# Optimization experiments

Measured on AMD Instinct MI355X. Metric: run time of the kernel, lower is better.

## Reference

```python
import jax, jax.numpy as jnp
import numpy as np

THRESH = 0.3
DECAY = 0.5


def spike_fn(x):
    # Heaviside threshold (forward only)
    return (x > THRESH).astype(x.dtype)


def setup_inputs() -> dict:
    key = jax.random.key(0)
    k_in, k0, k1, k2 = jax.random.split(key, 4)
    B, D0, T = 128, 512, 512
    inputs = jax.random.uniform(k_in, (B, D0, T), dtype=jnp.float32)
    w0 = jax.random.normal(k0, (512, 1024), dtype=jnp.float32)
    w1 = jax.random.normal(k1, (1024, 1024), dtype=jnp.float32)
    w2 = jax.random.normal(k2, (1024, 512), dtype=jnp.float32)
    return {"inputs": inputs, "w0": w0, "w1": w1, "w2": w2}


def reference(inputs, w0, w1, w2):
    ws = (w0, w1, w2)
    B = inputs.shape[0]
    layer_dims = tuple(w.shape[1] for w in ws)

    # time-major: [T, B, D0]
    xs = jnp.transpose(inputs, (2, 0, 1))

    mem0 = tuple(jnp.zeros((B, d), dtype=inputs.dtype) for d in layer_dims)
    spk0 = tuple(jnp.zeros((B, d), dtype=inputs.dtype) for d in layer_dims)

    def step(carry, x_t):
        mems, spikes = carry
        prev_spike = x_t  # layer-0 spikes come straight from the input
        new_mems, new_spikes = [], []
        for i, w in enumerate(ws):
            # leaky integrate with reset-by-spike, then fire
            mem = mems[i] * DECAY * (1.0 - spikes[i]) + prev_spike @ w
            s = spike_fn(mem)
            new_mems.append(mem)
            new_spikes.append(s)
            prev_spike = s
        return (tuple(new_mems), tuple(new_spikes)), None

    (_, spikes_final), _ = jax.lax.scan(step, (mem0, spk0), xs)
    return spikes_final[-1]
```

## Files before the change

kernel.cpp:

```cpp
#include <hip/hip_runtime.h>


typedef __bf16 bf16;
typedef __attribute__((ext_vector_type(8))) __bf16 bf16x8;
typedef __attribute__((ext_vector_type(16))) float f32x16;
typedef unsigned long long u64;

#define B_   128
#define D0_  512
#define T_   512
#define TS_  128
#define N1_  1024
#define N2_  1024
#define N3_  512
#define MFMA32(a,b,c) __builtin_amdgcn_mfma_f32_32x32x16_bf16((a),(b),(c),0,0,0)

#define GL2LDS(g, l) __builtin_amdgcn_global_load_lds( \
    (const __attribute__((address_space(1))) void*)(g), \
    (__attribute__((address_space(3))) void*)(l), 16, 0, 0)


__global__ __launch_bounds__(256)
void split_w(const float* __restrict__ W, bf16* __restrict__ WTh, bf16* __restrict__ WTl,
             int K, int N)
{
    __shared__ float tile[32][33];
    const int k0 = blockIdx.x * 32, n0 = blockIdx.y * 32;
    const int tx = threadIdx.x & 31, ty = threadIdx.x >> 5;
#pragma unroll
    for (int r = 0; r < 4; ++r)
        tile[ty + r * 8][tx] = W[(size_t)(k0 + ty + r * 8) * N + n0 + tx];
    __syncthreads();
#pragma unroll
    for (int r = 0; r < 4; ++r) {
        int nl = ty + r * 8;
        float v = tile[tx][nl];
        bf16 h = (bf16)v;
        size_t o = (size_t)(n0 + nl) * K + k0 + tx;
        WTh[o] = h;
        WTl[o] = (bf16)(v - (float)h);
    }
}

__global__ __launch_bounds__(256)
void split_x(const float* __restrict__ in, bf16* __restrict__ Xh, bf16* __restrict__ Xl)
{
    __shared__ float tile[32][33];
    const int b = blockIdx.z, d0 = blockIdx.x * 32, t0 = blockIdx.y * 32;
    const int tx = threadIdx.x & 31, ty = threadIdx.x >> 5;
#pragma unroll
    for (int r = 0; r < 4; ++r)
        tile[ty + r * 8][tx] = in[((size_t)b * D0_ + d0 + ty + r * 8) * T_ + t0 + tx];
    __syncthreads();
    const int s = t0 >> 7;
#pragma unroll
    for (int r = 0; r < 4; ++r) {
        int t  = t0 + ty + r * 8;
        int tl = t & (TS_ - 1);
        float v = tile[tx][ty + r * 8];
        bf16 h = (bf16)v;
        size_t o = (((size_t)s * B_ + b) * TS_ + tl) * D0_ + d0 + tx;
        Xh[o] = h;
        Xl[o] = (bf16)(v - (float)h);
    }
}

__device__ __forceinline__ bf16x8 expand8(unsigned v)
{
    union { unsigned u[4]; bf16x8 h; } r;
#pragma unroll
    for (int i = 0; i < 4; ++i) {
        r.u[i] = (((v >> (2 * i)) & 1u) ? 0x3F80u : 0u) |
                 (((v >> (2 * i + 1)) & 1u) ? 0x3F800000u : 0u);
    }
    return r.h;
}

__global__ __launch_bounds__(256)
void snn_layer0(const bf16* __restrict__ Ah, const bf16* __restrict__ Al,
                const bf16* __restrict__ WTh, const bf16* __restrict__ WTl,
                u64* __restrict__ bitsOut)
{
    constexpr int K = D0_;
    __shared__ char smem[32768];
    bf16* sAh = (bf16*)smem;
    bf16* sAl = (bf16*)(smem + 8192);
    bf16* sBh = (bf16*)(smem + 16384);
    bf16* sBl = (bf16*)(smem + 24576);
    float* If = (float*)smem;

    const int tid = threadIdx.x, lane = tid & 63, w = tid >> 6;
    const int wm = w & 1, wn = w >> 1;
    const int l31 = lane & 31, kh = lane >> 5;
    const int b = blockIdx.x;
    const int nb = blockIdx.y * 128;

    const int i4 = lane >> 2, c4 = lane & 3;
    const int csrc = c4 ^ ((i4 >> 1) & 3);
    const bf16* gBh = WTh + (size_t)(nb + w * 32 + i4) * K + csrc * 8;
    const bf16* gBl = WTl + (size_t)(nb + w * 32 + i4) * K + csrc * 8;
    bf16* lA  = sAh + w * 32 * 32;
    bf16* lAl = sAl + w * 32 * 32;
    bf16* lBh = sBh + w * 32 * 32;
    bf16* lBl = sBl + w * 32 * 32;

    int rA[2], rB[2], swA[2], swB[2];
#pragma unroll
    for (int i = 0; i < 2; ++i) {
        rA[i] = wm * 64 + i * 32 + l31;
        rB[i] = wn * 64 + i * 32 + l31;
        swA[i] = (rA[i] >> 1) & 3;
        swB[i] = (rB[i] >> 1) & 3;
    }

    float cm = 0.f, cs = 0.f;
    const int scol = tid & 63;
    float* Ifb = If + (tid >> 6) * 4096;

#pragma unroll 1
    for (int s = 0; s < T_ / TS_; ++s) {
        const size_t arow = ((size_t)s * B_ + b) * TS_;
        const bf16* gA  = Ah + (arow + w * 32 + i4) * K + csrc * 8;
        const bf16* gAl = Al + (arow + w * 32 + i4) * K + csrc * 8;

        f32x16 acc[2][2] = {};

#pragma unroll 1
        for (int ks = 0; ks < K / 32; ++ks) {
            const int go = ks * 32;
            __syncthreads();
#pragma unroll
            for (int inst = 0; inst < 2; ++inst) {
                GL2LDS(gA  + (size_t)inst * 16 * K + go, lA  + inst * 16 * 32);
                GL2LDS(gAl + (size_t)inst * 16 * K + go, lAl + inst * 16 * 32);
                GL2LDS(gBh + (size_t)inst * 16 * K + go, lBh + inst * 16 * 32);
                GL2LDS(gBl + (size_t)inst * 16 * K + go, lBl + inst * 16 * 32);
            }
            __syncthreads();

            bf16x8 a[2][2], al2[2][2];
#pragma unroll
            for (int mi = 0; mi < 2; ++mi)
#pragma unroll
                for (int h = 0; h < 2; ++h) {
                    const int off = rA[mi] * 32 + (((2 * h + kh) ^ swA[mi]) * 8);
                    a[mi][h]   = *(const bf16x8*)(sAh + off);
                    al2[mi][h] = *(const bf16x8*)(sAl + off);
                }
#pragma unroll
            for (int ni = 0; ni < 2; ++ni) {
#pragma unroll
                for (int h = 0; h < 2; ++h) {
                    const int off = rB[ni] * 32 + (((2 * h + kh) ^ swB[ni]) * 8);
                    bf16x8 bh = *(const bf16x8*)(sBh + off);
                    bf16x8 bl = *(const bf16x8*)(sBl + off);
#pragma unroll
                    for (int mi = 0; mi < 2; ++mi) {
                        acc[mi][ni] = MFMA32(a[mi][h], bh, acc[mi][ni]);
                        acc[mi][ni] = MFMA32(al2[mi][h], bh, acc[mi][ni]);
                        acc[mi][ni] = MFMA32(a[mi][h], bl, acc[mi][ni]);
                    }
                }
            }
        }

        u64 word0 = 0, word1 = 0;
        __syncthreads();
        if (wm == 0) {
#pragma unroll
            for (int ni = 0; ni < 2; ++ni)
#pragma unroll
                for (int mi = 0; mi < 2; ++mi)
#pragma unroll
                    for (int r = 0; r < 16; ++r) {
                        const int tt = mi * 32 + (r & 3) + 8 * (r >> 2) + 4 * kh;
                        If[wn * 4096 + tt * 64 + ni * 32 + l31] = acc[mi][ni][r];
                    }
        }
        __syncthreads();
        if (tid < 128) {
            float m = cm, sp = cs;
#pragma unroll 4
            for (int tt = 0; tt < 64; ++tt) {
                m = m * 0.5f * (1.0f - sp) + Ifb[tt * 64 + scol];
                const bool fire = m > 0.3f;
                sp = fire ? 1.0f : 0.0f;
                u64 bal = __ballot(fire);
                if ((tid & 63) == tt) word0 = bal;
            }
            cm = m; cs = sp;
        }
        __syncthreads();
        if (wm == 1) {
#pragma unroll
            for (int ni = 0; ni < 2; ++ni)
#pragma unroll
                for (int mi = 0; mi < 2; ++mi)
#pragma unroll
                    for (int r = 0; r < 16; ++r) {
                        const int tt = mi * 32 + (r & 3) + 8 * (r >> 2) + 4 * kh;
                        If[wn * 4096 + tt * 64 + ni * 32 + l31] = acc[mi][ni][r];
                    }
        }
        __syncthreads();
        if (tid < 128) {
            float m = cm, sp = cs;
#pragma unroll 4
            for (int tt = 0; tt < 64; ++tt) {
                m = m * 0.5f * (1.0f - sp) + Ifb[tt * 64 + scol];
                const bool fire = m > 0.3f;
                sp = fire ? 1.0f : 0.0f;
                u64 bal = __ballot(fire);
                if ((tid & 63) == tt) word1 = bal;
            }
            cm = m; cs = sp;
            u64* dst = bitsOut + ((size_t)s * B_ + b) * 2048;
            const int j8 = (nb >> 6) + (tid >> 6);
            const int t0 = tid & 63, t1 = 64 + (tid & 63);
            dst[t0 * 16 + (j8 ^ (t0 & 15))] = word0;
            dst[t1 * 16 + (j8 ^ (t1 & 15))] = word1;
        }
    }
}

template<bool WRITE_BITS>
__global__ __launch_bounds__(256, 3)
void snn_layer_bits(const u64* __restrict__ bitsIn,
                    const bf16* __restrict__ WTh, const bf16* __restrict__ WTl,
                    u64* __restrict__ bitsOut, float* __restrict__ outp, int N)
{
    constexpr int K = 1024;
    __shared__ char smem[49152];
    char* bitsLds = smem;
    bf16* sBh = (bf16*)(smem + 16384);
    bf16* sBl = (bf16*)(smem + 32768);
    float* If  = (float*)(smem + 16384);

    const int tid = threadIdx.x, lane = tid & 63, w = tid >> 6;
    const int wm = w & 1, wn = w >> 1;
    const int l31 = lane & 31, kh = lane >> 5;
    const int b = blockIdx.x;
    const int nb = blockIdx.y * 128;

    const int i8 = lane >> 3, c8 = lane & 7;
    const bf16* gBh = WTh + (size_t)(nb + w * 32 + i8) * K + (c8 ^ i8) * 8;
    const bf16* gBl = WTl + (size_t)(nb + w * 32 + i8) * K + (c8 ^ i8) * 8;
    bf16* lBh = sBh + (w * 32) * 64;
    bf16* lBl = sBl + (w * 32) * 64;

    int rA[2], rB[2];
#pragma unroll
    for (int i = 0; i < 2; ++i) {
        rA[i] = wm * 64 + i * 32 + l31;
        rB[i] = wn * 64 + i * 32 + l31;
    }
    const int sw7 = l31 & 7, sw15 = l31 & 15;

    float cm = 0.f, cs = 0.f;
    const int scol = tid & 63;
    float* Ifb = If + (tid >> 6) * 4096;

#pragma unroll 1
    for (int s = 0; s < T_ / TS_; ++s) {
        {
            const char* src = (const char*)bitsIn + ((size_t)s * B_ + b) * 16384;
#pragma unroll
            for (int i = 0; i < 4; ++i)
                GL2LDS(src + (w * 4 + i) * 1024 + lane * 16,
                       bitsLds + (w * 4 + i) * 1024);
        }

        f32x16 acc[2][2] = {};

#pragma unroll 1
        for (int ks = 0; ks < K / 64; ++ks) {
            const int go = ks * 64;
            __syncthreads();
#pragma unroll
            for (int inst = 0; inst < 4; ++inst) {
                GL2LDS(gBh + (size_t)(inst * 8) * K + go, lBh + inst * 8 * 64);
                GL2LDS(gBl + (size_t)(inst * 8) * K + go, lBl + inst * 8 * 64);
            }
            __syncthreads();

            u64 wA0 = *(const u64*)(bitsLds + rA[0] * 128 + ((ks ^ sw15) << 3)) >> (8 * kh);
            u64 wA1 = *(const u64*)(bitsLds + rA[1] * 128 + ((ks ^ sw15) << 3)) >> (8 * kh);

#pragma unroll
            for (int h = 0; h < 4; ++h) {
                bf16x8 a0 = expand8((unsigned)(wA0 >> (16 * h)) & 0xFFu);
                bf16x8 a1 = expand8((unsigned)(wA1 >> (16 * h)) & 0xFFu);
#pragma unroll
                for (int ni = 0; ni < 2; ++ni) {
                    const int off = rB[ni] * 64 + (((2 * h + kh) ^ sw7) << 3);
                    bf16x8 bh = *(const bf16x8*)(sBh + off);
                    bf16x8 bl = *(const bf16x8*)(sBl + off);
                    acc[0][ni] = MFMA32(a0, bh, acc[0][ni]);
                    acc[0][ni] = MFMA32(a0, bl, acc[0][ni]);
                    acc[1][ni] = MFMA32(a1, bh, acc[1][ni]);
                    acc[1][ni] = MFMA32(a1, bl, acc[1][ni]);
                }
            }
        }

        u64 word0 = 0, word1 = 0;
        __syncthreads();
        if (wm == 0) {
#pragma unroll
            for (int ni = 0; ni < 2; ++ni)
#pragma unroll
                for (int mi = 0; mi < 2; ++mi)
#pragma unroll
                    for (int r = 0; r < 16; ++r) {
                        const int tt = mi * 32 + (r & 3) + 8 * (r >> 2) + 4 * kh;
                        If[wn * 4096 + tt * 64 + ni * 32 + l31] = acc[mi][ni][r];
                    }
        }
        __syncthreads();
        if (tid < 128) {
            float m = cm, sp = cs;
#pragma unroll 4
            for (int tt = 0; tt < 64; ++tt) {
                m = m * 0.5f * (1.0f - sp) + Ifb[tt * 64 + scol];
                const bool fire = m > 0.3f;
                sp = fire ? 1.0f : 0.0f;
                if constexpr (WRITE_BITS) {
                    u64 bal = __ballot(fire);
                    if ((tid & 63) == tt) word0 = bal;
                }
            }
            cm = m; cs = sp;
        }
        __syncthreads();
        if (wm == 1) {
#pragma unroll
            for (int ni = 0; ni < 2; ++ni)
#pragma unroll
                for (int mi = 0; mi < 2; ++mi)
#pragma unroll
                    for (int r = 0; r < 16; ++r) {
                        const int tt = mi * 32 + (r & 3) + 8 * (r >> 2) + 4 * kh;
                        If[wn * 4096 + tt * 64 + ni * 32 + l31] = acc[mi][ni][r];
                    }
        }
        __syncthreads();
        if (tid < 128) {
            float m = cm, sp = cs;
#pragma unroll 4
            for (int tt = 0; tt < 64; ++tt) {
                m = m * 0.5f * (1.0f - sp) + Ifb[tt * 64 + scol];
                const bool fire = m > 0.3f;
                sp = fire ? 1.0f : 0.0f;
                if constexpr (WRITE_BITS) {
                    u64 bal = __ballot(fire);
                    if ((tid & 63) == tt) word1 = bal;
                }
            }
            cm = m; cs = sp;
            if constexpr (WRITE_BITS) {
                u64* dst = bitsOut + ((size_t)s * B_ + b) * 2048;
                const int j8 = (nb >> 6) + (tid >> 6);
                const int t0 = tid & 63, t1 = 64 + (tid & 63);
                dst[t0 * 16 + (j8 ^ (t0 & 15))] = word0;
                dst[t1 * 16 + (j8 ^ (t1 & 15))] = word1;
            } else {
                if (s == T_ / TS_ - 1)
                    outp[(size_t)b * N + nb + tid] = cs;
            }
        }
    }
}

extern "C" void kernel_launch(void* const* d_in, const int* in_sizes, int n_in,
                              void* d_out, int out_size, void* d_ws, size_t ws_size,
                              hipStream_t stream)
{
    const float* x  = (const float*)d_in[0];
    const float* w0 = (const float*)d_in[1];
    const float* w1 = (const float*)d_in[2];
    const float* w2 = (const float*)d_in[3];
    float* out = (float*)d_out;

    char* p = (char*)d_ws;
    bf16* w0h = (bf16*)p;  p += (size_t)N1_ * D0_ * 2;
    bf16* w0l = (bf16*)p;  p += (size_t)N1_ * D0_ * 2;
    bf16* w1h = (bf16*)p;  p += (size_t)N2_ * N1_ * 2;
    bf16* w1l = (bf16*)p;  p += (size_t)N2_ * N1_ * 2;
    bf16* w2h = (bf16*)p;  p += (size_t)N3_ * N2_ * 2;
    bf16* w2l = (bf16*)p;  p += (size_t)N3_ * N2_ * 2;
    bf16* Xh  = (bf16*)p;  p += (size_t)T_ * B_ * D0_ * 2;
    bf16* Xl  = (bf16*)p;  p += (size_t)T_ * B_ * D0_ * 2;
    u64* bits0 = (u64*)p;  p += (size_t)(T_/TS_) * B_ * TS_ * (N1_/8);
    u64* bits1 = (u64*)p;  p += (size_t)(T_/TS_) * B_ * TS_ * (N2_/8);

    split_w<<<dim3(D0_/32, N1_/32), 256, 0, stream>>>(w0, w0h, w0l, D0_, N1_);
    split_w<<<dim3(N1_/32, N2_/32), 256, 0, stream>>>(w1, w1h, w1l, N1_, N2_);
    split_w<<<dim3(N2_/32, N3_/32), 256, 0, stream>>>(w2, w2h, w2l, N2_, N3_);
    split_x<<<dim3(D0_/32, T_/32, B_), 256, 0, stream>>>(x, Xh, Xl);

    snn_layer0<<<dim3(B_, N1_/128), 256, 0, stream>>>(Xh, Xl, w0h, w0l, bits0);
    snn_layer_bits<true ><<<dim3(B_, N2_/128), 256, 0, stream>>>(
        bits0, w1h, w1l, bits1, nullptr, N2_);
    snn_layer_bits<false><<<dim3(B_, N3_/128), 256, 0, stream>>>(
        bits1, w2h, w2l, nullptr, out, N3_);
}
```

Baseline: 823.1 us.

## Double-buffer LDS tiles in layer GEMM kernels and simplify bit expansion

Converts the K-loops of the layer-0 and bit-input layer kernels to double-buffered LDS staging. The next tile's global-to-LDS loads are issued before the MFMAs on the current tile, so memory latency overlaps with compute and each step needs one barrier instead of two. Shared memory per block doubles (64KB and 80KB), and launch bounds drop occupancy to 2 blocks per CU. The spike-bit expansion into bf16 vectors is also rewritten as a multiply-and-mask trick instead of per-bit selects.

Result: faster. 804.2 us (-2.3%).

```diff
diff --git a/kernel.cpp b/kernel.cpp
--- a/kernel.cpp
+++ b/kernel.cpp
@@ -19,6 +19,10 @@
     (const __attribute__((address_space(1))) void*)(g), \
     (__attribute__((address_space(3))) void*)(l), 16, 0, 0)
 
+#define WAIT_BARRIER() do { \
+    asm volatile("s_waitcnt vmcnt(0)" ::: "memory"); \
+    __builtin_amdgcn_s_barrier(); } while (0)
+
 
 __global__ __launch_bounds__(256)
 void split_w(const float* __restrict__ W, bf16* __restrict__ WTh, bf16* __restrict__ WTl,
@@ -68,26 +72,29 @@
 __device__ __forceinline__ bf16x8 expand8(unsigned v)
 {
     union { unsigned u[4]; bf16x8 h; } r;
-#pragma unroll
-    for (int i = 0; i < 4; ++i) {
-        r.u[i] = (((v >> (2 * i)) & 1u) ? 0x3F80u : 0u) |
-                 (((v >> (2 * i + 1)) & 1u) ? 0x3F800000u : 0u);
-    }
+    const unsigned p = v * 0x8001u;
+#pragma unroll
+    for (int i = 0; i < 4; ++i)
+        r.u[i] = ((p >> (2 * i)) & 0x10001u) * 0x3F80u;
     return r.h;
 }
 
-__global__ __launch_bounds__(256)
+__global__ __launch_bounds__(256, 2)
 void snn_layer0(const bf16* __restrict__ Ah, const bf16* __restrict__ Al,
                 const bf16* __restrict__ WTh, const bf16* __restrict__ WTl,
                 u64* __restrict__ bitsOut)
 {
     constexpr int K = D0_;
-    __shared__ char smem[32768];
-    bf16* sAh = (bf16*)smem;
-    bf16* sAl = (bf16*)(smem + 8192);
-    bf16* sBh = (bf16*)(smem + 16384);
-    bf16* sBl = (bf16*)(smem + 24576);
-    float* If = (float*)smem;
+    __shared__ char smem[65536];
+    bf16* sA0  = (bf16*)(smem);
+    bf16* sAl0 = (bf16*)(smem + 8192);
+    bf16* sB0  = (bf16*)(smem + 16384);
+    bf16* sBl0 = (bf16*)(smem + 24576);
+    bf16* sA1  = (bf16*)(smem + 32768);
+    bf16* sAl1 = (bf16*)(smem + 40960);
+    bf16* sB1  = (bf16*)(smem + 49152);
+    bf16* sBl1 = (bf16*)(smem + 57344);
+    float* If  = (float*)smem;
 
     const int tid = threadIdx.x, lane = tid & 63, w = tid >> 6;
     const int wm = w & 1, wn = w >> 1;
@@ -99,10 +106,7 @@
     const int csrc = c4 ^ ((i4 >> 1) & 3);
     const bf16* gBh = WTh + (size_t)(nb + w * 32 + i4) * K + csrc * 8;
     const bf16* gBl = WTl + (size_t)(nb + w * 32 + i4) * K + csrc * 8;
-    bf16* lA  = sAh + w * 32 * 32;
-    bf16* lAl = sAl + w * 32 * 32;
-    bf16* lBh = sBh + w * 32 * 32;
-    bf16* lBl = sBl + w * 32 * 32;
+    const int wT = w * 32 * 32;
 
     int rA[2], rB[2], swA[2], swB[2];
 #pragma unroll
@@ -117,55 +121,67 @@
     const int scol = tid & 63;
     float* Ifb = If + (tid >> 6) * 4096;
 
+#define STAGE0(dA, dAl, dBh, dBl, go)                                          \
+    do {                                                                       \
+        _Pragma("unroll")                                                      \
+        for (int inst = 0; inst < 2; ++inst) {                                 \
+            GL2LDS(gA  + (size_t)(inst * 16) * K + (go), (dA)  + wT + inst * 16 * 32); \
+            GL2LDS(gAl + (size_t)(inst * 16) * K + (go), (dAl) + wT + inst * 16 * 32); \
+            GL2LDS(gBh + (size_t)(inst * 16) * K + (go), (dBh) + wT + inst * 16 * 32); \
+            GL2LDS(gBl + (size_t)(inst * 16) * K + (go), (dBl) + wT + inst * 16 * 32); \
+        }                                                                      \
+    } while (0)
+
+#define KSTEP0(cA, cAl, cBh, cBl)                                              \
+    do {                                                                       \
+        bf16x8 a[2][2], al2[2][2];                                             \
+        _Pragma("unroll")                                                      \
+        for (int mi = 0; mi < 2; ++mi)                                         \
+            _Pragma("unroll")                                                  \
+            for (int h = 0; h < 2; ++h) {                                      \
+                const int off = rA[mi] * 32 + (((2 * h + kh) ^ swA[mi]) * 8);  \
+                a[mi][h]   = *(const bf16x8*)((cA) + off);                     \
+                al2[mi][h] = *(const bf16x8*)((cAl) + off);                    \
+            }                                                                  \
+        _Pragma("unroll")                                                      \
+        for (int ni = 0; ni < 2; ++ni) {                                       \
+            _Pragma("unroll")                                                  \
+            for (int h = 0; h < 2; ++h) {                                      \
+                const int off = rB[ni] * 32 + (((2 * h + kh) ^ swB[ni]) * 8);  \
+                bf16x8 bh = *(const bf16x8*)((cBh) + off);                     \
+                bf16x8 bl = *(const bf16x8*)((cBl) + off);                     \
+                _Pragma("unroll")                                              \
+                for (int mi = 0; mi < 2; ++mi) {                               \
+                    acc[mi][ni] = MFMA32(a[mi][h], bh, acc[mi][ni]);           \
+                    acc[mi][ni] = MFMA32(al2[mi][h], bh, acc[mi][ni]);         \
+                    acc[mi][ni] = MFMA32(a[mi][h], bl, acc[mi][ni]);           \
+                }                                                              \
+            }                                                                  \
+        }                                                                      \
+        WAIT_BARRIER();                                                        \
+    } while (0)
+
 #pragma unroll 1
     for (int s = 0; s < T_ / TS_; ++s) {
         const size_t arow = ((size_t)s * B_ + b) * TS_;
         const bf16* gA  = Ah + (arow + w * 32 + i4) * K + csrc * 8;
         const bf16* gAl = Al + (arow + w * 32 + i4) * K + csrc * 8;
 
+        STAGE0(sA0, sAl0, sB0, sBl0, 0);
+        WAIT_BARRIER();
+
         f32x16 acc[2][2] = {};
 
 #pragma unroll 1
-        for (int ks = 0; ks < K / 32; ++ks) {
-            const int go = ks * 32;
-            __syncthreads();
-#pragma unroll
-            for (int inst = 0; inst < 2; ++inst) {
-                GL2LDS(gA  + (size_t)inst * 16 * K + go, lA  + inst * 16 * 32);
-                GL2LDS(gAl + (size_t)inst * 16 * K + go, lAl + inst * 16 * 32);
-                GL2LDS(gBh + (size_t)inst * 16 * K + go, lBh + inst * 16 * 32);
-                GL2LDS(gBl + (size_t)inst * 16 * K + go, lBl + inst * 16 * 32);
-            }
-            __syncthreads();
-
-            bf16x8 a[2][2], al2[2][2];
-#pragma unroll
-            for (int mi = 0; mi < 2; ++mi)
-#pragma unroll
-                for (int h = 0; h < 2; ++h) {
-                    const int off = rA[mi] * 32 + (((2 * h + kh) ^ swA[mi]) * 8);
-                    a[mi][h]   = *(const bf16x8*)(sAh + off);
-                    al2[mi][h] = *(const bf16x8*)(sAl + off);
-                }
-#pragma unroll
-            for (int ni = 0; ni < 2; ++ni) {
-#pragma unroll
-                for (int h = 0; h < 2; ++h) {
-                    const int off = rB[ni] * 32 + (((2 * h + kh) ^ swB[ni]) * 8);
-                    bf16x8 bh = *(const bf16x8*)(sBh + off);
-                    bf16x8 bl = *(const bf16x8*)(sBl + off);
-#pragma unroll
-                    for (int mi = 0; mi < 2; ++mi) {
-                        acc[mi][ni] = MFMA32(a[mi][h], bh, acc[mi][ni]);
-                        acc[mi][ni] = MFMA32(al2[mi][h], bh, acc[mi][ni]);
-                        acc[mi][ni] = MFMA32(a[mi][h], bl, acc[mi][ni]);
-                    }
-                }
-            }
+        for (int ks = 0; ks < K / 32; ks += 2) {
+            STAGE0(sA1, sAl1, sB1, sBl1, (ks + 1) * 32);
+            KSTEP0(sA0, sAl0, sB0, sBl0);
+            if (ks + 2 < K / 32)
+                STAGE0(sA0, sAl0, sB0, sBl0, (ks + 2) * 32);
+            KSTEP0(sA1, sAl1, sB1, sBl1);
         }
 
         u64 word0 = 0, word1 = 0;
-        __syncthreads();
         if (wm == 0) {
 #pragma unroll
             for (int ni = 0; ni < 2; ++ni)
@@ -220,20 +236,25 @@
             dst[t0 * 16 + (j8 ^ (t0 & 15))] = word0;
             dst[t1 * 16 + (j8 ^ (t1 & 15))] = word1;
         }
-    }
+        __syncthreads();
+    }
+#undef STAGE0
+#undef KSTEP0
 }
 
 template<bool WRITE_BITS>
-__global__ __launch_bounds__(256, 3)
+__global__ __launch_bounds__(256, 2)
 void snn_layer_bits(const u64* __restrict__ bitsIn,
                     const bf16* __restrict__ WTh, const bf16* __restrict__ WTl,
                     u64* __restrict__ bitsOut, float* __restrict__ outp, int N)
 {
     constexpr int K = 1024;
-    __shared__ char smem[49152];
+    __shared__ char smem[81920];
     char* bitsLds = smem;
-    bf16* sBh = (bf16*)(smem + 16384);
-    bf16* sBl = (bf16*)(smem + 32768);
+    bf16* sBh0 = (bf16*)(smem + 16384);
+    bf16* sBl0 = (bf16*)(smem + 32768);
+    bf16* sBh1 = (bf16*)(smem + 49152);
+    bf16* sBl1 = (bf16*)(smem + 65536);
     float* If  = (float*)(smem + 16384);
 
     const int tid = threadIdx.x, lane = tid & 63, w = tid >> 6;
@@ -245,8 +266,7 @@
     const int i8 = lane >> 3, c8 = lane & 7;
     const bf16* gBh = WTh + (size_t)(nb + w * 32 + i8) * K + (c8 ^ i8) * 8;
     const bf16* gBl = WTl + (size_t)(nb + w * 32 + i8) * K + (c8 ^ i8) * 8;
-    bf16* lBh = sBh + (w * 32) * 64;
-    bf16* lBl = sBl + (w * 32) * 64;
+    const int wB = w * 32 * 64;
 
     int rA[2], rB[2];
 #pragma unroll
@@ -254,11 +274,42 @@
         rA[i] = wm * 64 + i * 32 + l31;
         rB[i] = wn * 64 + i * 32 + l31;
     }
-    const int sw7 = l31 & 7, sw15 = l31 & 15;
+    const int sw7 = l31 & 7, sw15 = l31 & 15, sh8 = 8 * kh;
 
     float cm = 0.f, cs = 0.f;
     const int scol = tid & 63;
     float* Ifb = If + (tid >> 6) * 4096;
+
+#define STAGEB(dBh, dBl, go)                                                   \
+    do {                                                                       \
+        _Pragma("unroll")                                                      \
+        for (int inst = 0; inst < 4; ++inst) {                                 \
+            GL2LDS(gBh + (size_t)(inst * 8) * K + (go), (dBh) + wB + inst * 8 * 64); \
+            GL2LDS(gBl + (size_t)(inst * 8) * K + (go), (dBl) + wB + inst * 8 * 64); \
+        }                                                                      \
+    } while (0)
+
+#define KSTEPB(ks, cBh, cBl)                                                   \
+    do {                                                                       \
+        u64 wA0 = *(const u64*)(bitsLds + rA[0] * 128 + (((ks) ^ sw15) << 3)) >> sh8; \
+        u64 wA1 = *(const u64*)(bitsLds + rA[1] * 128 + (((ks) ^ sw15) << 3)) >> sh8; \
+        _Pragma("unroll")                                                      \
+        for (int h = 0; h < 4; ++h) {                                          \
+            bf16x8 a0 = expand8((unsigned)(wA0 >> (16 * h)) & 0xFFu);          \
+            bf16x8 a1 = expand8((unsigned)(wA1 >> (16 * h)) & 0xFFu);          \
+            _Pragma("unroll")                                                  \
+            for (int ni = 0; ni < 2; ++ni) {                                   \
+                const int off = rB[ni] * 64 + (((2 * h + kh) ^ sw7) << 3);     \
+                bf16x8 bh = *(const bf16x8*)((cBh) + off);                     \
+                bf16x8 bl = *(const bf16x8*)((cBl) + off);                     \
+                acc[0][ni] = MFMA32(a0, bh, acc[0][ni]);                       \
+                acc[0][ni] = MFMA32(a0, bl, acc[0][ni]);                       \
+                acc[1][ni] = MFMA32(a1, bh, acc[1][ni]);                       \
+                acc[1][ni] = MFMA32(a1, bl, acc[1][ni]);                       \
+            }                                                                  \
+        }                                                                      \
+        WAIT_BARRIER();                                                        \
+    } while (0)
 
 #pragma unroll 1
     for (int s = 0; s < T_ / TS_; ++s) {
@@ -269,42 +320,21 @@
                 GL2LDS(src + (w * 4 + i) * 1024 + lane * 16,
                        bitsLds + (w * 4 + i) * 1024);
         }
+        STAGEB(sBh0, sBl0, 0);
+        WAIT_BARRIER();
 
         f32x16 acc[2][2] = {};
 
 #pragma unroll 1
-        for (int ks = 0; ks < K / 64; ++ks) {
-            const int go = ks * 64;
-            __syncthreads();
-#pragma unroll
-            for (int inst = 0; inst < 4; ++inst) {
-                GL2LDS(gBh + (size_t)(inst * 8) * K + go, lBh + inst * 8 * 64);
-                GL2LDS(gBl + (size_t)(inst * 8) * K + go, lBl + inst * 8 * 64);
-            }
-            __syncthreads();
-
-            u64 wA0 = *(const u64*)(bitsLds + rA[0] * 128 + ((ks ^ sw15) << 3)) >> (8 * kh);
-            u64 wA1 = *(const u64*)(bitsLds + rA[1] * 128 + ((ks ^ sw15) << 3)) >> (8 * kh);
-
-#pragma unroll
-            for (int h = 0; h < 4; ++h) {
-                bf16x8 a0 = expand8((unsigned)(wA0 >> (16 * h)) & 0xFFu);
-                bf16x8 a1 = expand8((unsigned)(wA1 >> (16 * h)) & 0xFFu);
-#pragma unroll
-                for (int ni = 0; ni < 2; ++ni) {
-                    const int off = rB[ni] * 64 + (((2 * h + kh) ^ sw7) << 3);
-                    bf16x8 bh = *(const bf16x8*)(sBh + off);
-                    bf16x8 bl = *(const bf16x8*)(sBl + off);
-                    acc[0][ni] = MFMA32(a0, bh, acc[0][ni]);
-                    acc[0][ni] = MFMA32(a0, bl, acc[0][ni]);
-                    acc[1][ni] = MFMA32(a1, bh, acc[1][ni]);
-                    acc[1][ni] = MFMA32(a1, bl, acc[1][ni]);
-                }
-            }
+        for (int ks = 0; ks < K / 64; ks += 2) {
+            STAGEB(sBh1, sBl1, (ks + 1) * 64);
+            KSTEPB(ks, sBh0, sBl0);
+            if (ks + 2 < K / 64)
+                STAGEB(sBh0, sBl0, (ks + 2) * 64);
+            KSTEPB(ks + 1, sBh1, sBl1);
         }
 
         u64 word0 = 0, word1 = 0;
-        __syncthreads();
         if (wm == 0) {
 #pragma unroll
             for (int ni = 0; ni < 2; ++ni)
@@ -368,7 +398,10 @@
                     outp[(size_t)b * N + nb + tid] = cs;
             }
         }
-    }
+        __syncthreads();
+    }
+#undef STAGEB
+#undef KSTEPB
 }
 
 extern "C" void kernel_launch(void* const* d_in, const int* in_sizes, int n_in,
```
